# Optimization experiments

Hardware: AMD Instinct MI355X
Metric: run time of the kernel (lower is better)

## Reference

```python
import jax, jax.numpy as jnp
import numpy as np

B, S, D_IN, D_OUT = 4, 2048, 1024, 1024

def setup_inputs() -> dict:
    key = jax.random.key(0)
    kx, kq, kk, kv = jax.random.split(key, 4)
    sc = 1.0 / np.sqrt(D_IN)
    x = jax.random.normal(kx, (B, S, D_IN), dtype=jnp.float32)
    Wq = jax.random.normal(kq, (D_IN, D_OUT), dtype=jnp.float32) * sc
    Wk = jax.random.normal(kk, (D_IN, D_OUT), dtype=jnp.float32) * sc
    Wv = jax.random.normal(kv, (D_IN, D_OUT), dtype=jnp.float32) * sc
    return {"x": x, "Wq": Wq, "Wk": Wk, "Wv": Wv}

def reference(x, Wq, Wk, Wv):
    # x: [B,S,Din]; projections to [B,S,Dout]
    q = jnp.einsum('bsd,de->bse', x, Wq)
    k = jnp.einsum('bsd,de->bse', x, Wk)
    v = jnp.einsum('bsd,de->bse', x, Wv)
    scale = 1.0 / jnp.sqrt(jnp.asarray(q.shape[-1], q.dtype))
    scores = jnp.einsum('bqe,bke->bqk', q, k) * scale  # [B,S,S]
    causal = jnp.tril(jnp.ones((scores.shape[-2], scores.shape[-1]), dtype=bool))
    scores = jnp.where(causal, scores, -jnp.inf)
    attn = jax.nn.softmax(scores, axis=-1)
    # dropout p=0.0 -> identity
    return jnp.einsum('bqk,bke->bqe', attn, v)
```

## Files before the change

### kernel.cpp

```cpp
#include <hip/hip_runtime.h>

#define SEQ 2048
#define DIM 1024

typedef __attribute__((ext_vector_type(8))) __bf16 bf16x8;
typedef __attribute__((ext_vector_type(4))) float f32x4;

typedef __attribute__((address_space(1))) unsigned char gu8_t;
typedef __attribute__((address_space(3))) unsigned char lu8_t;

__device__ __forceinline__ void async_copy16(const void* g, void* l) {
  __builtin_amdgcn_global_load_lds((gu8_t*)g, (lu8_t*)l, 16, 0, 0);
}

__device__ __forceinline__ ushort f2bf(float f) {
  union { float f; unsigned u; } v;
  v.f = f;
  unsigned r = v.u + 0x7FFFu + ((v.u >> 16) & 1u);
  return (ushort)(r >> 16);
}

__global__ void detect_dtype(const unsigned* __restrict__ words,
                             int* __restrict__ flag) {
  const int t = threadIdx.x;
  int hits = 0;
  for (int i = 0; i < 64; i++) {
    const unsigned w = words[t * 64 + i];
    const unsigned b = (w >> 8) & 0x7Fu;
    hits += (b >= 0x3Bu && b <= 0x42u) ? 1 : 0;
  }
#pragma unroll
  for (int o = 32; o > 0; o >>= 1) hits += __shfl_xor(hits, o, 64);
  if (t == 0) *flag = (hits > 2048) ? 1 : 0;
}

__global__ void convert_x(const void* __restrict__ in,
                          ushort* __restrict__ out,
                          const int* __restrict__ flag, int n8) {
  const int i = blockIdx.x * 256 + threadIdx.x;
  if (i >= n8) return;
  if (*flag) {
    reinterpret_cast<uint4*>(out)[i] = reinterpret_cast<const uint4*>(in)[i];
  } else {
    const float4* f = reinterpret_cast<const float4*>(in);
    const float4 a = f[2 * i], b = f[2 * i + 1];
    ushort4 lo, hi;
    lo.x = f2bf(a.x); lo.y = f2bf(a.y); lo.z = f2bf(a.z); lo.w = f2bf(a.w);
    hi.x = f2bf(b.x); hi.y = f2bf(b.y); hi.z = f2bf(b.z); hi.w = f2bf(b.w);
    reinterpret_cast<ushort4*>(out)[2 * i] = lo;
    reinterpret_cast<ushort4*>(out)[2 * i + 1] = hi;
  }
}

__global__ void transpose_w(const void* __restrict__ w0,
                            const void* __restrict__ w1,
                            const void* __restrict__ w2,
                            ushort* __restrict__ out,
                            const int* __restrict__ flag) {
  __shared__ ushort tile[64][68];
  const int z = blockIdx.z;
  const void* in = (z == 0) ? w0 : (z == 1) ? w1 : w2;
  ushort* op = out + (size_t)z * 1024 * 1024;
  const int c0 = blockIdx.x * 64, r0 = blockIdx.y * 64;
  const int t = threadIdx.x;
  if (*flag) {
    const ushort* ip = (const ushort*)in;
#pragma unroll
    for (int i = 0; i < 4; i++) {
      const int lin = i * 256 + t;
      const int r = lin >> 4, c4 = (lin & 15) << 2;
      const ushort4 v = *reinterpret_cast<const ushort4*>(
          ip + (size_t)(r0 + r) * 1024 + c0 + c4);
      tile[r][c4 + 0] = v.x; tile[r][c4 + 1] = v.y;
      tile[r][c4 + 2] = v.z; tile[r][c4 + 3] = v.w;
    }
  } else {
    const float* ip = (const float*)in;
#pragma unroll
    for (int i = 0; i < 4; i++) {
      const int lin = i * 256 + t;
      const int r = lin >> 4, c4 = (lin & 15) << 2;
      const float4 v = *reinterpret_cast<const float4*>(
          ip + (size_t)(r0 + r) * 1024 + c0 + c4);
      tile[r][c4 + 0] = f2bf(v.x); tile[r][c4 + 1] = f2bf(v.y);
      tile[r][c4 + 2] = f2bf(v.z); tile[r][c4 + 3] = f2bf(v.w);
    }
  }
  __syncthreads();
#pragma unroll
  for (int i = 0; i < 4; i++) {
    const int lin = i * 256 + t;
    const int c = lin >> 4, r4 = (lin & 15) << 2;
    ushort4 v;
    v.x = tile[r4 + 0][c]; v.y = tile[r4 + 1][c];
    v.z = tile[r4 + 2][c]; v.w = tile[r4 + 3][c];
    *reinterpret_cast<ushort4*>(op + (size_t)(c0 + c) * 1024 + r0 + r4) = v;
  }
}

__global__ void transpose_bf16(const ushort* __restrict__ in,
                               ushort* __restrict__ out, int R, int C,
                               long inZ, long outZ) {
  __shared__ ushort tile[64][68];
  const ushort* ip = in + (size_t)blockIdx.z * inZ;
  ushort* op = out + (size_t)blockIdx.z * outZ;
  const int c0 = blockIdx.x * 64, r0 = blockIdx.y * 64;
  const int t = threadIdx.x;
#pragma unroll
  for (int i = 0; i < 4; i++) {
    const int lin = i * 256 + t;
    const int r = lin >> 4, c4 = (lin & 15) << 2;
    const ushort4 v =
        *reinterpret_cast<const ushort4*>(ip + (size_t)(r0 + r) * C + c0 + c4);
    tile[r][c4 + 0] = v.x; tile[r][c4 + 1] = v.y;
    tile[r][c4 + 2] = v.z; tile[r][c4 + 3] = v.w;
  }
  __syncthreads();
#pragma unroll
  for (int i = 0; i < 4; i++) {
    const int lin = i * 256 + t;
    const int c = lin >> 4, r4 = (lin & 15) << 2;
    ushort4 v;
    v.x = tile[r4 + 0][c]; v.y = tile[r4 + 1][c];
    v.z = tile[r4 + 2][c]; v.w = tile[r4 + 3][c];
    *reinterpret_cast<ushort4*>(op + (size_t)(c0 + c) * R + r0 + r4) = v;
  }
}

__global__ __launch_bounds__(256, 4) void gemm_bt(
    const ushort* __restrict__ A, const ushort* __restrict__ Bt,
    void* __restrict__ Cv, const int* __restrict__ flag, int M, int N, int K,
    long aZ, long bZ, long cZ, int zBase, float scale0, float scale1,
    int triSkip, int causalK, int outKind) {
  __shared__ ushort lA[128 * 32];
  __shared__ ushort lB[128 * 32];

  const int nT = gridDim.x;
  const int id = blockIdx.y * nT + blockIdx.x;
  const int xcd = id & 7;
  const int loc = id >> 3;
  const int n0 = (loc % nT) * 128;
  const int m0 = (xcd + ((loc / nT) << 3)) * 128;
  if (triSkip && n0 > m0 + 127) return;

  const ushort* Ab = A + (size_t)blockIdx.z * aZ;
  const ushort* Bb = Bt + (size_t)blockIdx.z * bZ;

  const int t = threadIdx.x;
  const int lane = t & 63;
  const int w = t >> 6;
  const int wm = (w >> 1) * 64;
  const int wn = (w & 1) * 64;
  const int quad = lane >> 4;
  const int l15 = lane & 15;

  f32x4 acc[4][4] = {};

  const int kEnd = causalK ? ((m0 + 128 < K) ? (m0 + 128) : K) : K;

  const int idx0 = t;
  const int idx1 = t + 256;
  const int rowA0 = idx0 >> 2, colA0 = (idx0 & 3) << 3;
  const int rowA1 = idx1 >> 2, colA1 = (idx1 & 3) << 3;

  for (int k0 = 0; k0 < kEnd; k0 += 32) {
    __syncthreads();
    async_copy16(Ab + (size_t)(m0 + rowA0) * K + k0 + colA0, lA + idx0 * 8);
    async_copy16(Ab + (size_t)(m0 + rowA1) * K + k0 + colA1, lA + idx1 * 8);
    async_copy16(Bb + (size_t)(n0 + rowA0) * K + k0 + colA0, lB + idx0 * 8);
    async_copy16(Bb + (size_t)(n0 + rowA1) * K + k0 + colA1, lB + idx1 * 8);
    __syncthreads();

    bf16x8 af[4], bfr[4];
#pragma unroll
    for (int mi = 0; mi < 4; mi++)
      af[mi] = *(const bf16x8*)(lA + (wm + mi * 16 + l15) * 32 + quad * 8);
#pragma unroll
    for (int ni = 0; ni < 4; ni++)
      bfr[ni] = *(const bf16x8*)(lB + (wn + ni * 16 + l15) * 32 + quad * 8);
#pragma unroll
    for (int mi = 0; mi < 4; mi++)
#pragma unroll
      for (int ni = 0; ni < 4; ni++)
        acc[mi][ni] = __builtin_amdgcn_mfma_f32_16x16x32_bf16(
            af[mi], bfr[ni], acc[mi][ni], 0, 0, 0);
  }

  const float scale = (blockIdx.z == 0 && zBase == 0) ? scale0 : scale1;
  const bool storeBf = (outKind == 1) || (outKind == 2 && *flag != 0);
  const size_t zc = (size_t)(zBase + blockIdx.z) * cZ;
#pragma unroll
  for (int mi = 0; mi < 4; mi++)
#pragma unroll
    for (int ni = 0; ni < 4; ni++)
#pragma unroll
      for (int r = 0; r < 4; r++) {
        const int row = m0 + wm + mi * 16 + quad * 4 + r;
        const int col = n0 + wn + ni * 16 + l15;
        const float vv = acc[mi][ni][r] * scale;
        if (storeBf) {
          ushort* C = (ushort*)Cv + zc;
          C[(size_t)row * N + col] = f2bf(vv);
        } else {
          float* C = (float*)Cv + zc;
          C[(size_t)row * N + col] = vv;
        }
      }
}

__global__ void softmax_causal(const float* __restrict__ Sc,
                               ushort* __restrict__ P) {
  const int rid = blockIdx.x;
  const int i = rid & (SEQ - 1);
  const float* row = Sc + (size_t)rid * SEQ;
  ushort* prow = P + (size_t)rid * SEQ;
  const int t = threadIdx.x;
  __shared__ float red[4];

  float r[8];
  float mx = -3.0e38f;
#pragma unroll
  for (int it = 0; it < 8; it++) {
    const int j = it * 256 + t;
    r[it] = (j <= i) ? row[j] : -3.0e38f;
    mx = fmaxf(mx, r[it]);
  }
#pragma unroll
  for (int o = 32; o > 0; o >>= 1) mx = fmaxf(mx, __shfl_xor(mx, o, 64));
  if ((t & 63) == 0) red[t >> 6] = mx;
  __syncthreads();
  mx = fmaxf(fmaxf(red[0], red[1]), fmaxf(red[2], red[3]));
  __syncthreads();

  float sum = 0.0f;
#pragma unroll
  for (int it = 0; it < 8; it++) {
    r[it] = __expf(r[it] - mx);
    sum += r[it];
  }
#pragma unroll
  for (int o = 32; o > 0; o >>= 1) sum += __shfl_xor(sum, o, 64);
  if ((t & 63) == 0) red[t >> 6] = sum;
  __syncthreads();
  sum = red[0] + red[1] + red[2] + red[3];
  const float inv = 1.0f / sum;

#pragma unroll
  for (int it = 0; it < 8; it++) {
    const int j = it * 256 + t;
    prow[j] = f2bf(r[it] * inv);
  }
}

extern "C" void kernel_launch(void* const* d_in, const int* in_sizes, int n_in,
                              void* d_out, int out_size, void* d_ws,
                              size_t ws_size, hipStream_t stream) {
  char* ws = (char*)d_ws;
  const size_t MB = 1024 * 1024;
  int* flag = (int*)ws;
  ushort* wt = (ushort*)(ws + 1 * MB);
  ushort* xb = (ushort*)(ws + 7 * MB);
  ushort* q = (ushort*)(ws + 23 * MB);
  ushort* kk = (ushort*)(ws + 39 * MB);
  ushort* v = (ushort*)(ws + 55 * MB);
  ushort* vt = (ushort*)(ws + 71 * MB);
  float* sc = (float*)(ws + 87 * MB);

  int g = 4;
  while (g > 1 && (87 + 24 * (size_t)g) * MB > ws_size) g >>= 1;
  ushort* p = (ushort*)(ws + (87 + 16 * (size_t)g) * MB);
  (void)kk;

  detect_dtype<<<dim3(1), 64, 0, stream>>>((const unsigned*)d_in[0], flag);

  convert_x<<<dim3(4096), 256, 0, stream>>>(d_in[0], xb, flag,
                                            (8192 * 1024) / 8);

  transpose_w<<<dim3(16, 16, 3), 256, 0, stream>>>(d_in[1], d_in[2], d_in[3],
                                                   wt, flag);

  gemm_bt<<<dim3(8, 64, 3), 256, 0, stream>>>(
      xb, wt, (void*)q, flag, 8192, 1024, 1024, 0L, (long)1024 * 1024,
      (long)8192 * 1024, 0, 0.03125f, 1.0f, 0, 0, 1);

  transpose_bf16<<<dim3(16, 32, 4), 256, 0, stream>>>(
      v, vt, 2048, 1024, (long)SEQ * DIM, (long)DIM * SEQ);

  for (int b0 = 0; b0 < 4; b0 += g) {
    gemm_bt<<<dim3(16, 16, g), 256, 0, stream>>>(
        q + (size_t)b0 * SEQ * DIM, kk + (size_t)b0 * SEQ * DIM, (void*)sc,
        flag, 2048, 2048, 1024, (long)SEQ * DIM, (long)SEQ * DIM,
        (long)SEQ * SEQ, 0, 1.0f, 1.0f, 1, 0, 0);
    softmax_causal<<<dim3(g * SEQ), 256, 0, stream>>>(sc, p);
    gemm_bt<<<dim3(8, 16, g), 256, 0, stream>>>(
        p, vt + (size_t)b0 * DIM * SEQ, d_out, flag, 2048, 1024, 2048,
        (long)SEQ * SEQ, (long)DIM * SEQ, (long)SEQ * DIM, b0, 1.0f, 1.0f, 0,
        1, 2);
  }
}
```

Measured before the change: 274.9 us.

## Store scores in bf16 and fuse softmax normalization into the PV GEMM

Attention scores are now written as bf16 instead of fp32. A lightweight pass computes only per-row max and inverse sum. The PV GEMM recomputes exp and normalization while staging the score tile into LDS, so the separate probability matrix is never materialized. This cuts memory traffic for the S×S intermediates and removes the per-batch group loop, at the cost of extra exp work inside the GEMM, a synchronous (non-async) load path for the A tile, and reduced precision in the stored scores.

```diff
diff --git a/kernel.cpp b/kernel.cpp
--- a/kernel.cpp
+++ b/kernel.cpp
@@ -18,6 +18,13 @@
   v.f = f;
   unsigned r = v.u + 0x7FFFu + ((v.u >> 16) & 1u);
   return (ushort)(r >> 16);
+}
+
+__device__ __forceinline__ float bf2f_lo(unsigned u) {
+  return __uint_as_float(u << 16);
+}
+__device__ __forceinline__ float bf2f_hi(unsigned u) {
+  return __uint_as_float(u & 0xFFFF0000u);
 }
 
 __global__ void detect_dtype(const unsigned* __restrict__ words,
@@ -131,7 +138,7 @@
     const ushort* __restrict__ A, const ushort* __restrict__ Bt,
     void* __restrict__ Cv, const int* __restrict__ flag, int M, int N, int K,
     long aZ, long bZ, long cZ, int zBase, float scale0, float scale1,
-    int triSkip, int causalK, int outKind) {
+    int triSkip, int outKind) {
   __shared__ ushort lA[128 * 32];
   __shared__ ushort lB[128 * 32];
 
@@ -156,14 +163,12 @@
 
   f32x4 acc[4][4] = {};
 
-  const int kEnd = causalK ? ((m0 + 128 < K) ? (m0 + 128) : K) : K;
-
   const int idx0 = t;
   const int idx1 = t + 256;
   const int rowA0 = idx0 >> 2, colA0 = (idx0 & 3) << 3;
   const int rowA1 = idx1 >> 2, colA1 = (idx1 & 3) << 3;
 
-  for (int k0 = 0; k0 < kEnd; k0 += 32) {
+  for (int k0 = 0; k0 < K; k0 += 32) {
     __syncthreads();
     async_copy16(Ab + (size_t)(m0 + rowA0) * K + k0 + colA0, lA + idx0 * 8);
     async_copy16(Ab + (size_t)(m0 + rowA1) * K + k0 + colA1, lA + idx1 * 8);
@@ -208,22 +213,24 @@
       }
 }
 
-__global__ void softmax_causal(const float* __restrict__ Sc,
-                               ushort* __restrict__ P) {
+__global__ void softmax_stats(const ushort* __restrict__ Sc,
+                              float2* __restrict__ stats) {
   const int rid = blockIdx.x;
   const int i = rid & (SEQ - 1);
-  const float* row = Sc + (size_t)rid * SEQ;
-  ushort* prow = P + (size_t)rid * SEQ;
+  const ushort* row = Sc + (size_t)rid * SEQ;
   const int t = threadIdx.x;
   __shared__ float red[4];
 
   float r[8];
   float mx = -3.0e38f;
 #pragma unroll
-  for (int it = 0; it < 8; it++) {
-    const int j = it * 256 + t;
-    r[it] = (j <= i) ? row[j] : -3.0e38f;
-    mx = fmaxf(mx, r[it]);
+  for (int it = 0; it < 4; it++) {
+    const int j = it * 512 + 2 * t;
+    unsigned u = 0;
+    if (j <= i) u = *reinterpret_cast<const unsigned*>(row + j);
+    r[2 * it] = (j <= i) ? bf2f_lo(u) : -3.0e38f;
+    r[2 * it + 1] = (j + 1 <= i) ? bf2f_hi(u) : -3.0e38f;
+    mx = fmaxf(mx, fmaxf(r[2 * it], r[2 * it + 1]));
   }
 #pragma unroll
   for (int o = 32; o > 0; o >>= 1) mx = fmaxf(mx, __shfl_xor(mx, o, 64));
@@ -234,22 +241,117 @@
 
   float sum = 0.0f;
 #pragma unroll
-  for (int it = 0; it < 8; it++) {
-    r[it] = __expf(r[it] - mx);
-    sum += r[it];
-  }
+  for (int it = 0; it < 8; it++) sum += __expf(r[it] - mx);
 #pragma unroll
   for (int o = 32; o > 0; o >>= 1) sum += __shfl_xor(sum, o, 64);
   if ((t & 63) == 0) red[t >> 6] = sum;
   __syncthreads();
   sum = red[0] + red[1] + red[2] + red[3];
-  const float inv = 1.0f / sum;
-
-#pragma unroll
-  for (int it = 0; it < 8; it++) {
-    const int j = it * 256 + t;
-    prow[j] = f2bf(r[it] * inv);
-  }
+  if (t == 0) stats[rid] = make_float2(mx, 1.0f / sum);
+}
+
+__global__ __launch_bounds__(256, 4) void gemm_pv(
+    const ushort* __restrict__ Sc, const ushort* __restrict__ Vt,
+    const float2* __restrict__ stats, void* __restrict__ Cv,
+    const int* __restrict__ flag, long cZ) {
+  __shared__ ushort lA[128 * 32];
+  __shared__ ushort lB[128 * 32];
+  __shared__ float2 st_s[128];
+
+  const int N = DIM, K = SEQ;
+  const int nT = gridDim.x;
+  const int id = blockIdx.y * nT + blockIdx.x;
+  const int xcd = id & 7;
+  const int loc = id >> 3;
+  const int n0 = (loc % nT) * 128;
+  const int m0 = (xcd + ((loc / nT) << 3)) * 128;
+
+  const ushort* Ab = Sc + (size_t)blockIdx.z * SEQ * SEQ;
+  const ushort* Bb = Vt + (size_t)blockIdx.z * (size_t)DIM * SEQ;
+
+  const int t = threadIdx.x;
+  const int lane = t & 63;
+  const int w = t >> 6;
+  const int wm = (w >> 1) * 64;
+  const int wn = (w & 1) * 64;
+  const int quad = lane >> 4;
+  const int l15 = lane & 15;
+
+  if (t < 128) st_s[t] = stats[(size_t)blockIdx.z * SEQ + m0 + t];
+
+  f32x4 acc[4][4] = {};
+
+  const int kEnd = m0 + 128;
+
+  const int idx0 = t;
+  const int idx1 = t + 256;
+  const int rowA0 = idx0 >> 2, colA0 = (idx0 & 3) << 3;
+  const int rowA1 = idx1 >> 2, colA1 = (idx1 & 3) << 3;
+
+  for (int k0 = 0; k0 < kEnd; k0 += 32) {
+    __syncthreads();
+    async_copy16(Bb + (size_t)(n0 + rowA0) * K + k0 + colA0, lB + idx0 * 8);
+    async_copy16(Bb + (size_t)(n0 + rowA1) * K + k0 + colA1, lB + idx1 * 8);
+#pragma unroll
+    for (int c = 0; c < 2; c++) {
+      const int idx = (c == 0) ? idx0 : idx1;
+      const int row = (c == 0) ? rowA0 : rowA1;
+      const int col = (c == 0) ? colA0 : colA1;
+      const int q = m0 + row;
+      const float2 st = st_s[row];
+      const uint4 s4 = *reinterpret_cast<const uint4*>(
+          Ab + (size_t)q * K + k0 + col);
+      const unsigned words[4] = {s4.x, s4.y, s4.z, s4.w};
+      uint4 o4;
+      unsigned ow[4];
+#pragma unroll
+      for (int jj = 0; jj < 4; jj++) {
+        const int kb = k0 + col + 2 * jj;
+        const float p0 =
+            (kb <= q) ? __expf(bf2f_lo(words[jj]) - st.x) * st.y : 0.0f;
+        const float p1 =
+            (kb + 1 <= q) ? __expf(bf2f_hi(words[jj]) - st.x) * st.y : 0.0f;
+        ow[jj] = (unsigned)f2bf(p0) | ((unsigned)f2bf(p1) << 16);
+      }
+      o4.x = ow[0]; o4.y = ow[1]; o4.z = ow[2]; o4.w = ow[3];
+      *reinterpret_cast<uint4*>(lA + idx * 8) = o4;
+    }
+    __syncthreads();
+
+    bf16x8 af[4], bfr[4];
+#pragma unroll
+    for (int mi = 0; mi < 4; mi++)
+      af[mi] = *(const bf16x8*)(lA + (wm + mi * 16 + l15) * 32 + quad * 8);
+#pragma unroll
+    for (int ni = 0; ni < 4; ni++)
+      bfr[ni] = *(const bf16x8*)(lB + (wn + ni * 16 + l15) * 32 + quad * 8);
+#pragma unroll
+    for (int mi = 0; mi < 4; mi++)
+#pragma unroll
+      for (int ni = 0; ni < 4; ni++)
+        acc[mi][ni] = __builtin_amdgcn_mfma_f32_16x16x32_bf16(
+            af[mi], bfr[ni], acc[mi][ni], 0, 0, 0);
+  }
+
+  const bool storeBf = (*flag != 0);
+  const size_t zc = (size_t)blockIdx.z * cZ;
+#pragma unroll
+  for (int mi = 0; mi < 4; mi++)
+#pragma unroll
+    for (int ni = 0; ni < 4; ni++)
+#pragma unroll
+      for (int r = 0; r < 4; r++) {
+        const int row = m0 + wm + mi * 16 + quad * 4 + r;
+        const int col = n0 + wn + ni * 16 + l15;
+        const float vv = acc[mi][ni][r];
+        if (storeBf) {
+          ushort* C = (ushort*)Cv + zc;
+          C[(size_t)row * N + col] = f2bf(vv);
+        } else {
+          float* C = (float*)Cv + zc;
+          C[(size_t)row * N + col] = vv;
+        }
+      }
 }
 
 extern "C" void kernel_launch(void* const* d_in, const int* in_sizes, int n_in,
@@ -264,11 +366,8 @@
   ushort* kk = (ushort*)(ws + 39 * MB);
   ushort* v = (ushort*)(ws + 55 * MB);
   ushort* vt = (ushort*)(ws + 71 * MB);
-  float* sc = (float*)(ws + 87 * MB);
-
-  int g = 4;
-  while (g > 1 && (87 + 24 * (size_t)g) * MB > ws_size) g >>= 1;
-  ushort* p = (ushort*)(ws + (87 + 16 * (size_t)g) * MB);
+  ushort* sc = (ushort*)(ws + 87 * MB);
+  float2* stats = (float2*)(ws + 119 * MB);
   (void)kk;
 
   detect_dtype<<<dim3(1), 64, 0, stream>>>((const unsigned*)d_in[0], flag);
@@ -281,20 +380,17 @@
 
   gemm_bt<<<dim3(8, 64, 3), 256, 0, stream>>>(
       xb, wt, (void*)q, flag, 8192, 1024, 1024, 0L, (long)1024 * 1024,
-      (long)8192 * 1024, 0, 0.03125f, 1.0f, 0, 0, 1);
+      (long)8192 * 1024, 0, 0.03125f, 1.0f, 0, 1);
 
   transpose_bf16<<<dim3(16, 32, 4), 256, 0, stream>>>(
       v, vt, 2048, 1024, (long)SEQ * DIM, (long)DIM * SEQ);
 
-  for (int b0 = 0; b0 < 4; b0 += g) {
-    gemm_bt<<<dim3(16, 16, g), 256, 0, stream>>>(
-        q + (size_t)b0 * SEQ * DIM, kk + (size_t)b0 * SEQ * DIM, (void*)sc,
-        flag, 2048, 2048, 1024, (long)SEQ * DIM, (long)SEQ * DIM,
-        (long)SEQ * SEQ, 0, 1.0f, 1.0f, 1, 0, 0);
-    softmax_causal<<<dim3(g * SEQ), 256, 0, stream>>>(sc, p);
-    gemm_bt<<<dim3(8, 16, g), 256, 0, stream>>>(
-        p, vt + (size_t)b0 * DIM * SEQ, d_out, flag, 2048, 1024, 2048,
-        (long)SEQ * SEQ, (long)DIM * SEQ, (long)SEQ * DIM, b0, 1.0f, 1.0f, 0,
-        1, 2);
-  }
-}
+  gemm_bt<<<dim3(16, 16, 4), 256, 0, stream>>>(
+      q, kk, (void*)sc, flag, 2048, 2048, 1024, (long)SEQ * DIM,
+      (long)SEQ * DIM, (long)SEQ * SEQ, 0, 1.0f, 1.0f, 1, 1);
+
+  softmax_stats<<<dim3(4 * SEQ), 256, 0, stream>>>(sc, stats);
+
+  gemm_pv<<<dim3(8, 16, 4), 256, 0, stream>>>(sc, vt, stats, d_out, flag,
+                                              (long)SEQ * DIM);
+}
```

New measurement: 315.1 us. +14.6%, slower.

## Store attention scores in bf16, balance causal tiles, run all batches at once

Applied to the files above, without the earlier changes.

The QK^T GEMM now writes scores as bf16 instead of fp32. The softmax kernel reads and writes packed bf16 pairs, which halves the score-matrix traffic. A new causalBal tile mapping pairs low and high row tiles per XCD so skipped upper-triangle tiles are spread evenly across XCDs. The batch-group loop is removed, and all four batches launch in single kernels using fixed workspace offsets. The risks are lower score precision before softmax and a larger fixed workspace requirement.

```diff
diff --git a/kernel.cpp b/kernel.cpp
--- a/kernel.cpp
+++ b/kernel.cpp
@@ -18,6 +18,13 @@
   v.f = f;
   unsigned r = v.u + 0x7FFFu + ((v.u >> 16) & 1u);
   return (ushort)(r >> 16);
+}
+
+__device__ __forceinline__ float bf2f_lo(unsigned u) {
+  return __uint_as_float(u << 16);
+}
+__device__ __forceinline__ float bf2f_hi(unsigned u) {
+  return __uint_as_float(u & 0xFFFF0000u);
 }
 
 __global__ void detect_dtype(const unsigned* __restrict__ words,
@@ -131,7 +138,7 @@
     const ushort* __restrict__ A, const ushort* __restrict__ Bt,
     void* __restrict__ Cv, const int* __restrict__ flag, int M, int N, int K,
     long aZ, long bZ, long cZ, int zBase, float scale0, float scale1,
-    int triSkip, int causalK, int outKind) {
+    int triSkip, int causalK, int causalBal, int outKind) {
   __shared__ ushort lA[128 * 32];
   __shared__ ushort lB[128 * 32];
 
@@ -139,8 +146,11 @@
   const int id = blockIdx.y * nT + blockIdx.x;
   const int xcd = id & 7;
   const int loc = id >> 3;
-  const int n0 = (loc % nT) * 128;
-  const int m0 = (xcd + ((loc / nT) << 3)) * 128;
+  const int nt = loc % nT;
+  const int mt = causalBal ? ((loc / nT == 0) ? xcd : ((int)gridDim.y - 1 - xcd))
+                           : (xcd + ((loc / nT) << 3));
+  const int n0 = nt * 128;
+  const int m0 = mt * 128;
   if (triSkip && n0 > m0 + 127) return;
 
   const ushort* Ab = A + (size_t)blockIdx.z * aZ;
@@ -208,11 +218,11 @@
       }
 }
 
-__global__ void softmax_causal(const float* __restrict__ Sc,
-                               ushort* __restrict__ P) {
+__global__ void softmax_p(const ushort* __restrict__ Sc,
+                          ushort* __restrict__ P) {
   const int rid = blockIdx.x;
   const int i = rid & (SEQ - 1);
-  const float* row = Sc + (size_t)rid * SEQ;
+  const ushort* row = Sc + (size_t)rid * SEQ;
   ushort* prow = P + (size_t)rid * SEQ;
   const int t = threadIdx.x;
   __shared__ float red[4];
@@ -220,10 +230,12 @@
   float r[8];
   float mx = -3.0e38f;
 #pragma unroll
-  for (int it = 0; it < 8; it++) {
-    const int j = it * 256 + t;
-    r[it] = (j <= i) ? row[j] : -3.0e38f;
-    mx = fmaxf(mx, r[it]);
+  for (int it = 0; it < 4; it++) {
+    const int j = it * 512 + 2 * t;
+    const unsigned u = *reinterpret_cast<const unsigned*>(row + j);
+    r[2 * it] = (j <= i) ? bf2f_lo(u) : -3.0e38f;
+    r[2 * it + 1] = (j + 1 <= i) ? bf2f_hi(u) : -3.0e38f;
+    mx = fmaxf(mx, fmaxf(r[2 * it], r[2 * it + 1]));
   }
 #pragma unroll
   for (int o = 32; o > 0; o >>= 1) mx = fmaxf(mx, __shfl_xor(mx, o, 64));
@@ -246,9 +258,11 @@
   const float inv = 1.0f / sum;
 
 #pragma unroll
-  for (int it = 0; it < 8; it++) {
-    const int j = it * 256 + t;
-    prow[j] = f2bf(r[it] * inv);
+  for (int it = 0; it < 4; it++) {
+    const int j = it * 512 + 2 * t;
+    const unsigned w = (unsigned)f2bf(r[2 * it] * inv) |
+                       ((unsigned)f2bf(r[2 * it + 1] * inv) << 16);
+    *reinterpret_cast<unsigned*>(prow + j) = w;
   }
 }
 
@@ -264,11 +278,8 @@
   ushort* kk = (ushort*)(ws + 39 * MB);
   ushort* v = (ushort*)(ws + 55 * MB);
   ushort* vt = (ushort*)(ws + 71 * MB);
-  float* sc = (float*)(ws + 87 * MB);
-
-  int g = 4;
-  while (g > 1 && (87 + 24 * (size_t)g) * MB > ws_size) g >>= 1;
-  ushort* p = (ushort*)(ws + (87 + 16 * (size_t)g) * MB);
+  ushort* sc = (ushort*)(ws + 87 * MB);
+  ushort* p = (ushort*)(ws + 119 * MB);
   (void)kk;
 
   detect_dtype<<<dim3(1), 64, 0, stream>>>((const unsigned*)d_in[0], flag);
@@ -281,20 +292,18 @@
 
   gemm_bt<<<dim3(8, 64, 3), 256, 0, stream>>>(
       xb, wt, (void*)q, flag, 8192, 1024, 1024, 0L, (long)1024 * 1024,
-      (long)8192 * 1024, 0, 0.03125f, 1.0f, 0, 0, 1);
+      (long)8192 * 1024, 0, 0.03125f, 1.0f, 0, 0, 0, 1);
 
   transpose_bf16<<<dim3(16, 32, 4), 256, 0, stream>>>(
       v, vt, 2048, 1024, (long)SEQ * DIM, (long)DIM * SEQ);
 
-  for (int b0 = 0; b0 < 4; b0 += g) {
-    gemm_bt<<<dim3(16, 16, g), 256, 0, stream>>>(
-        q + (size_t)b0 * SEQ * DIM, kk + (size_t)b0 * SEQ * DIM, (void*)sc,
-        flag, 2048, 2048, 1024, (long)SEQ * DIM, (long)SEQ * DIM,
-        (long)SEQ * SEQ, 0, 1.0f, 1.0f, 1, 0, 0);
-    softmax_causal<<<dim3(g * SEQ), 256, 0, stream>>>(sc, p);
-    gemm_bt<<<dim3(8, 16, g), 256, 0, stream>>>(
-        p, vt + (size_t)b0 * DIM * SEQ, d_out, flag, 2048, 1024, 2048,
-        (long)SEQ * SEQ, (long)DIM * SEQ, (long)SEQ * DIM, b0, 1.0f, 1.0f, 0,
-        1, 2);
-  }
-}
+  gemm_bt<<<dim3(16, 16, 4), 256, 0, stream>>>(
+      q, kk, (void*)sc, flag, 2048, 2048, 1024, (long)SEQ * DIM,
+      (long)SEQ * DIM, (long)SEQ * SEQ, 0, 1.0f, 1.0f, 1, 0, 1, 1);
+
+  softmax_p<<<dim3(4 * SEQ), 256, 0, stream>>>(sc, p);
+
+  gemm_bt<<<dim3(8, 16, 4), 256, 0, stream>>>(
+      p, vt, d_out, flag, 2048, 1024, 2048, (long)SEQ * SEQ, (long)DIM * SEQ,
+      (long)SEQ * DIM, 0, 1.0f, 1.0f, 0, 1, 1, 2);
+}
```

After: 275.3 us. No clear change (+0.1%).
